# Performance work log

Measured on AMD Instinct MI355X. Metric: run time of the kernel, lower is better.

## Reference

```python
import jax, jax.numpy as jnp
import numpy as np

B, A, C = 128, 8732, 21
ALPHA = 1.0
NEG_POS_RATIO = 3


def setup_inputs() -> dict:
    key = jax.random.key(0)
    k1, k2, k3, k4, k5 = jax.random.split(key, 5)
    confidences = jax.random.normal(k1, (B, A, C), dtype=jnp.float32)
    locations = jax.random.normal(k2, (B, A, 4), dtype=jnp.float32)
    gt_locations = jax.random.normal(k3, (B, A, 4), dtype=jnp.float32)
    raw_cls = jax.random.randint(k4, (B, A), 1, C)
    is_pos = jax.random.uniform(k5, (B, A)) < 0.03
    gt_labels = jnp.where(is_pos, raw_cls, 0).astype(jnp.int32)
    return {
        "confidences": confidences,
        "locations": locations,
        "gt_labels": gt_labels,
        "gt_locations": gt_locations,
    }


def reference(confidences, locations, gt_labels, gt_locations):
    pos_mask = gt_labels > 0                     # (B, A)
    neg_avail = gt_labels == 0                   # (B, A)

    # smooth L1 (beta=1) summed over positive anchors
    d = locations - gt_locations                 # (B, A, 4)
    ad = jnp.abs(d)
    sl1 = jnp.where(ad < 1.0, 0.5 * d * d, ad - 0.5)
    loc_loss = jnp.sum(sl1 * pos_mask[..., None].astype(sl1.dtype))

    # per-anchor cross entropy
    logp = jax.nn.log_softmax(confidences, axis=-1)              # (B, A, C)
    ce = -jnp.take_along_axis(logp, gt_labels[..., None].astype(jnp.int32), axis=-1)[..., 0]  # (B, A)

    # hard negative mining: top-(3*num_pos) CE among negatives, per row
    num_pos = jnp.sum(pos_mask, axis=1)                          # (B,)
    num_neg = jnp.minimum(NEG_POS_RATIO * num_pos, jnp.sum(neg_avail, axis=1))
    ce_neg = jnp.where(pos_mask, 0.0, ce)                        # zero out positives (CE >= 0)
    order = jnp.argsort(-ce_neg, axis=1)                         # descending
    ranks = jnp.argsort(order, axis=1)                           # rank of each anchor in descending order
    neg_mask = ranks < num_neg[:, None]

    keep = pos_mask | neg_mask
    conf_loss = jnp.sum(jnp.where(keep, ce, 0.0))

    total_loss = (loc_loss + ALPHA * conf_loss) / jnp.sum(num_pos).astype(loc_loss.dtype)
    return total_loss
```

## Files before the change

kernel.cpp:

```cpp
#include <hip/hip_runtime.h>
#include <math.h>

#define B_ 128
#define A_ 8732
#define C_ 21
#define TPB 1024
#define KPT 9
#define NT 9

typedef float f4u __attribute__((ext_vector_type(4), aligned(4)));

#define OFF_SCAL 0

__global__ __launch_bounds__(1024) void k_fused(
        const float* __restrict__ conf, const float* __restrict__ loc,
        const int* __restrict__ lab, const float* __restrict__ gloc,
        float* __restrict__ gsum, int* __restrict__ gN,
        int* __restrict__ gticket, float* __restrict__ out)
{
    __shared__ unsigned long long shCnt[2][16];
    __shared__ float shS[16];
    __shared__ float shL[16];
    __shared__ int   shC[16];
    __shared__ int   shNp;

    const int b    = blockIdx.x;
    const int tid  = threadIdx.x;
    const int wave = tid >> 6, lane = tid & 63;
    const size_t rowoff = (size_t)b * A_;

    unsigned keys[KPT];
    float pce = 0.f, lloss = 0.f;
    int pcnt = 0;

    #pragma unroll
    for (int t = 0; t < NT; ++t) {
        const int a  = t * TPB + tid;
        unsigned key = 0u;
        if (a < A_) {
            const int L = lab[rowoff + a];

            const float* vp = conf + (rowoff + a) * C_;
            float v[C_];
            #pragma unroll
            for (int q = 0; q < 5; ++q) {
                const f4u x = *(const f4u*)(vp + 4 * q);
                v[4*q+0] = x.x; v[4*q+1] = x.y; v[4*q+2] = x.z; v[4*q+3] = x.w;
            }
            v[20] = vp[20];

            float m = v[0];
            #pragma unroll
            for (int j = 1; j < C_; ++j) m = fmaxf(m, v[j]);
            float s = 0.f;
            #pragma unroll
            for (int j = 0; j < C_; ++j) s += __expf(v[j] - m);

            float vL = v[0];
            #pragma unroll
            for (int j = 1; j < C_; ++j) vL = (j == L) ? v[j] : vL;

            const float ce = __logf(s) + m - vL;
            if (L > 0) {
                pce += ce;
                pcnt++;
                const float4 lv = ((const float4*)loc)[rowoff + a];
                const float4 gv = ((const float4*)gloc)[rowoff + a];
                float dx = lv.x - gv.x, dy = lv.y - gv.y,
                      dz = lv.z - gv.z, dw = lv.w - gv.w;
                float ax = fabsf(dx), ay = fabsf(dy),
                      az = fabsf(dz), aw = fabsf(dw);
                lloss += (ax < 1.f) ? 0.5f * dx * dx : ax - 0.5f;
                lloss += (ay < 1.f) ? 0.5f * dy * dy : ay - 0.5f;
                lloss += (az < 1.f) ? 0.5f * dz * dz : az - 0.5f;
                lloss += (aw < 1.f) ? 0.5f * dw * dw : aw - 0.5f;
            } else {
                key = __float_as_uint(ce);
            }
        }
        keys[t] = key;
    }

    {
        float p = pce, l = lloss; int c = pcnt;
        #pragma unroll
        for (int off = 32; off > 0; off >>= 1) {
            p += __shfl_down(p, off);
            l += __shfl_down(l, off);
            c += __shfl_down(c, off);
        }
        if (lane == 0) { shS[wave] = p; shL[wave] = l; shC[wave] = c; }
    }
    __syncthreads();
    float rowsum = 0.f;
    if (tid == 0) {
        float P = 0.f, Lx = 0.f; int Cc = 0;
        #pragma unroll
        for (int w = 0; w < 16; ++w) { P += shS[w]; Lx += shL[w]; Cc += shC[w]; }
        shNp = Cc;
        rowsum = P + Lx;
    }
    __syncthreads();
    const int np = shNp;

    {
        unsigned c0 = 0; float s0 = 0.f;
        #pragma unroll
        for (int j = 0; j < KPT; ++j) {
            c0 += (unsigned)__popcll(__ballot(keys[j] != 0u));
            s0 += __uint_as_float(keys[j]);
        }
        #pragma unroll
        for (int off = 32; off > 0; off >>= 1) s0 += __shfl_down(s0, off);
        if (lane == 0) { shCnt[0][wave] = c0; shS[wave] = s0; }
    }
    __syncthreads();

    const int k = min(3 * np, A_ - np);
    unsigned cnt0 = 0; float sum0 = 0.f;
    #pragma unroll
    for (int w = 0; w < 16; ++w) { cnt0 += (unsigned)shCnt[0][w]; sum0 += shS[w]; }

    float negsum = 0.f;
    if (k <= 0) {
        negsum = 0.f;
    } else if (cnt0 < (unsigned)k) {
        negsum = sum0;
    } else {
        unsigned lo = 0u, hi = 0x42800000u;
        int p = 1;
        while (hi - lo > 1u) {
            const unsigned w = hi - lo;
            unsigned m1, m2, m3;
            if (w >= 4u) { const unsigned q = w >> 2; m1 = lo + q; m2 = lo + 2*q; m3 = lo + 3*q; }
            else         { m1 = m2 = m3 = lo + (w >> 1); }
            unsigned c1 = 0, c2 = 0, c3 = 0;
            #pragma unroll
            for (int j = 0; j < KPT; ++j) {
                c1 += (unsigned)__popcll(__ballot(keys[j] > m1));
                c2 += (unsigned)__popcll(__ballot(keys[j] > m2));
                c3 += (unsigned)__popcll(__ballot(keys[j] > m3));
            }
            if (lane == 0)
                shCnt[p][wave] = (unsigned long long)c1
                               | ((unsigned long long)c2 << 16)
                               | ((unsigned long long)c3 << 32);
            __syncthreads();
            unsigned long long tsum = 0;
            #pragma unroll
            for (int w2 = 0; w2 < 16; ++w2) tsum += shCnt[p][w2];
            const int C1 = (int)(tsum & 0xFFFF), C2 = (int)((tsum >> 16) & 0xFFFF),
                      C3 = (int)((tsum >> 32) & 0xFFFF);
            if      (C3 >= k) { lo = m3; }
            else if (C2 >= k) { lo = m2; hi = m3; }
            else if (C1 >= k) { lo = m1; hi = m2; }
            else              { hi = m1; }
            p ^= 1;
        }

        const unsigned kth = hi;
        unsigned c = 0; float s = 0.f;
        #pragma unroll
        for (int j = 0; j < KPT; ++j) {
            c += (unsigned)__popcll(__ballot(keys[j] > kth));
            s += (keys[j] > kth) ? __uint_as_float(keys[j]) : 0.f;
        }
        #pragma unroll
        for (int off = 32; off > 0; off >>= 1) s += __shfl_down(s, off);
        if (lane == 0) { shCnt[0][wave] = c; shS[wave] = s; }
        __syncthreads();
        if (tid == 0) {
            unsigned Cg = 0; float Sg = 0.f;
            #pragma unroll
            for (int w = 0; w < 16; ++w) { Cg += (unsigned)shCnt[0][w]; Sg += shS[w]; }
            negsum = Sg + (float)(k - (int)Cg) * __uint_as_float(kth);
        }
    }

    if (tid == 0) {
        atomicAdd(gsum, rowsum + negsum);
        atomicAdd(gN, np);
        __threadfence();
        const int t = atomicAdd(gticket, 1);
        if (t == B_ - 1) {
            const float S = atomicAdd(gsum, 0.f);
            const int   N = atomicAdd(gN, 0);
            out[0] = S / (float)N;
        }
    }
}

extern "C" void kernel_launch(void* const* d_in, const int* in_sizes, int n_in,
                              void* d_out, int out_size, void* d_ws, size_t ws_size,
                              hipStream_t stream) {
    const float* conf = (const float*)d_in[0];
    const float* loc  = (const float*)d_in[1];
    const int*   lab  = (const int*)d_in[2];
    const float* gloc = (const float*)d_in[3];

    char* ws = (char*)d_ws;
    float* gsum    = (float*)(ws + OFF_SCAL);
    int*   gN      = (int*)(ws + OFF_SCAL + 4);
    int*   gticket = (int*)(ws + OFF_SCAL + 8);

    hipMemsetAsync(ws + OFF_SCAL, 0, 12, stream);

    k_fused<<<B_, TPB, 0, stream>>>(conf, loc, lab, gloc,
                                    gsum, gN, gticket, (float*)d_out);
}
```

Before: 190.7 us.

## Software-pipeline anchor loads and use online softmax per float4 chunk

Prefetches the next tile's confidences, label, and location vectors into registers while the current tile is processed, so global memory latency overlaps with compute. Replaces the two-pass max/exp softmax with an online streaming softmax over float4 chunks. Loads loc/gloc unconditionally for every anchor instead of only for positives, and adds a launch-bounds occupancy hint. This raises register pressure and adds extra location traffic and extra exp work from rescaling.

After: 194.5 us. About the same (+2.0%).

```diff
diff --git a/kernel.cpp b/kernel.cpp
--- a/kernel.cpp
+++ b/kernel.cpp
@@ -12,7 +12,22 @@
 
 #define OFF_SCAL 0
 
-__global__ __launch_bounds__(1024) void k_fused(
+#define SM_CHUNK(X, BASE)                                             \
+    {                                                                 \
+        const float e0 = X.x, e1 = X.y, e2 = X.z, e3 = X.w;           \
+        const float cm = fmaxf(fmaxf(e0, e1), fmaxf(e2, e3));         \
+        const float nm = fmaxf(m, cm);                                \
+        s = s * __expf(m - nm)                                        \
+          + __expf(e0 - nm) + __expf(e1 - nm)                         \
+          + __expf(e2 - nm) + __expf(e3 - nm);                        \
+        m = nm;                                                       \
+        vL = (cL == (BASE) + 0) ? e0 : vL;                            \
+        vL = (cL == (BASE) + 1) ? e1 : vL;                            \
+        vL = (cL == (BASE) + 2) ? e2 : vL;                            \
+        vL = (cL == (BASE) + 3) ? e3 : vL;                            \
+    }
+
+__global__ __launch_bounds__(1024, 4) void k_fused(
         const float* __restrict__ conf, const float* __restrict__ loc,
         const int* __restrict__ lab, const float* __restrict__ gloc,
         float* __restrict__ gsum, int* __restrict__ gN,
@@ -33,41 +48,56 @@
     float pce = 0.f, lloss = 0.f;
     int pcnt = 0;
 
+    f4u cx0, cx1, cx2, cx3, cx4; float cxs; int cL; float4 clv, cgv;
+    f4u nx0, nx1, nx2, nx3, nx4; float nxs; int nL; float4 nlv, ngv;
+
+    {
+        const float* vp = conf + (rowoff + tid) * C_;
+        cx0 = *(const f4u*)(vp);      cx1 = *(const f4u*)(vp + 4);
+        cx2 = *(const f4u*)(vp + 8);  cx3 = *(const f4u*)(vp + 12);
+        cx4 = *(const f4u*)(vp + 16); cxs = vp[20];
+        cL  = lab[rowoff + tid];
+        clv = ((const float4*)loc)[rowoff + tid];
+        cgv = ((const float4*)gloc)[rowoff + tid];
+    }
+
     #pragma unroll
     for (int t = 0; t < NT; ++t) {
-        const int a  = t * TPB + tid;
+        if (t + 1 < NT) {
+            const int a = (t + 1) * TPB + tid;
+            if (a < A_) {
+                const float* vp = conf + (rowoff + a) * C_;
+                nx0 = *(const f4u*)(vp);      nx1 = *(const f4u*)(vp + 4);
+                nx2 = *(const f4u*)(vp + 8);  nx3 = *(const f4u*)(vp + 12);
+                nx4 = *(const f4u*)(vp + 16); nxs = vp[20];
+                nL  = lab[rowoff + a];
+                nlv = ((const float4*)loc)[rowoff + a];
+                ngv = ((const float4*)gloc)[rowoff + a];
+            } else {
+                nx0 = (f4u){0.f, 0.f, 0.f, 0.f}; nx1 = nx0; nx2 = nx0;
+                nx3 = nx0; nx4 = nx0; nxs = 0.f; nL = 0;
+                nlv = make_float4(0.f, 0.f, 0.f, 0.f); ngv = nlv;
+            }
+        }
+
+        const int a = t * TPB + tid;
         unsigned key = 0u;
         if (a < A_) {
-            const int L = lab[rowoff + a];
-
-            const float* vp = conf + (rowoff + a) * C_;
-            float v[C_];
-            #pragma unroll
-            for (int q = 0; q < 5; ++q) {
-                const f4u x = *(const f4u*)(vp + 4 * q);
-                v[4*q+0] = x.x; v[4*q+1] = x.y; v[4*q+2] = x.z; v[4*q+3] = x.w;
-            }
-            v[20] = vp[20];
-
-            float m = v[0];
-            #pragma unroll
-            for (int j = 1; j < C_; ++j) m = fmaxf(m, v[j]);
-            float s = 0.f;
-            #pragma unroll
-            for (int j = 0; j < C_; ++j) s += __expf(v[j] - m);
-
-            float vL = v[0];
-            #pragma unroll
-            for (int j = 1; j < C_; ++j) vL = (j == L) ? v[j] : vL;
-
+            float m = -1e30f, s = 0.f, vL = 0.f;
+            SM_CHUNK(cx0,  0) SM_CHUNK(cx1,  4) SM_CHUNK(cx2,  8)
+            SM_CHUNK(cx3, 12) SM_CHUNK(cx4, 16)
+            {
+                const float nm = fmaxf(m, cxs);
+                s = s * __expf(m - nm) + __expf(cxs - nm);
+                m = nm;
+                vL = (cL == 20) ? cxs : vL;
+            }
             const float ce = __logf(s) + m - vL;
-            if (L > 0) {
+            if (cL > 0) {
                 pce += ce;
                 pcnt++;
-                const float4 lv = ((const float4*)loc)[rowoff + a];
-                const float4 gv = ((const float4*)gloc)[rowoff + a];
-                float dx = lv.x - gv.x, dy = lv.y - gv.y,
-                      dz = lv.z - gv.z, dw = lv.w - gv.w;
+                float dx = clv.x - cgv.x, dy = clv.y - cgv.y,
+                      dz = clv.z - cgv.z, dw = clv.w - cgv.w;
                 float ax = fabsf(dx), ay = fabsf(dy),
                       az = fabsf(dz), aw = fabsf(dw);
                 lloss += (ax < 1.f) ? 0.5f * dx * dx : ax - 0.5f;
@@ -79,6 +109,9 @@
             }
         }
         keys[t] = key;
+
+        cx0 = nx0; cx1 = nx1; cx2 = nx2; cx3 = nx3; cx4 = nx4;
+        cxs = nxs; cL = nL; clv = nlv; cgv = ngv;
     }
 
     {
```

## Split fused loss into wide CE kernel and per-row selection kernel

Applied to the files above, without the earlier changes.

The single 128-block fused kernel is replaced by two kernels. The first computes per-anchor cross entropy and the localization loss over a (35, 128) grid of 256-thread blocks, so many more blocks share the memory-bound read of the confidences. It writes negative CE values to a workspace buffer and atomically accumulates per-row positive counts. The second kernel loads each row's CE values into shared memory and runs the existing radix-style top-k selection. This costs an extra ~4.5 MB write and read plus a second launch, and the softmax now uses an online max/sum form.

Measured after the change: 220.8 us. 1.16x slower.

```diff
diff --git a/kernel.cpp b/kernel.cpp
--- a/kernel.cpp
+++ b/kernel.cpp
@@ -4,111 +4,136 @@
 #define B_ 128
 #define A_ 8732
 #define C_ 21
+#define APB 256
+#define NBLK ((A_ + APB - 1) / APB)
 #define TPB 1024
 #define KPT 9
-#define NT 9
 
 typedef float f4u __attribute__((ext_vector_type(4), aligned(4)));
 
 #define OFF_SCAL 0
-
-__global__ __launch_bounds__(1024) void k_fused(
+#define OFF_RNP  16
+#define OFF_CEN  1024
+
+#define SM_CHUNK(X, BASE)                                             \
+    {                                                                 \
+        const float e0 = X.x, e1 = X.y, e2 = X.z, e3 = X.w;           \
+        const float cm = fmaxf(fmaxf(e0, e1), fmaxf(e2, e3));         \
+        const float nm = fmaxf(m, cm);                                \
+        s = s * __expf(m - nm)                                        \
+          + __expf(e0 - nm) + __expf(e1 - nm)                         \
+          + __expf(e2 - nm) + __expf(e3 - nm);                        \
+        m = nm;                                                       \
+        vL = (L == (BASE) + 0) ? e0 : vL;                             \
+        vL = (L == (BASE) + 1) ? e1 : vL;                             \
+        vL = (L == (BASE) + 2) ? e2 : vL;                             \
+        vL = (L == (BASE) + 3) ? e3 : vL;                             \
+    }
+
+__global__ __launch_bounds__(256) void k_ce(
         const float* __restrict__ conf, const float* __restrict__ loc,
         const int* __restrict__ lab, const float* __restrict__ gloc,
+        float* __restrict__ ce_neg, int* __restrict__ row_np,
+        float* __restrict__ gsum)
+{
+    const int row = blockIdx.y;
+    const int a   = blockIdx.x * APB + threadIdx.x;
+    const int tid = threadIdx.x;
+    const int wave = tid >> 6, lane = tid & 63;
+
+    float pce = 0.f, lloss = 0.f;
+    int pcnt = 0;
+
+    if (a < A_) {
+        const size_t idx = (size_t)row * A_ + a;
+        const int L = lab[idx];
+        const float* vp = conf + idx * C_;
+        const f4u x0 = *(const f4u*)(vp);
+        const f4u x1 = *(const f4u*)(vp + 4);
+        const f4u x2 = *(const f4u*)(vp + 8);
+        const f4u x3 = *(const f4u*)(vp + 12);
+        const f4u x4 = *(const f4u*)(vp + 16);
+        const float xs = vp[20];
+
+        float m = -1e30f, s = 0.f, vL = 0.f;
+        SM_CHUNK(x0,  0) SM_CHUNK(x1,  4) SM_CHUNK(x2,  8)
+        SM_CHUNK(x3, 12) SM_CHUNK(x4, 16)
+        {
+            const float nm = fmaxf(m, xs);
+            s = s * __expf(m - nm) + __expf(xs - nm);
+            m = nm;
+            vL = (L == 20) ? xs : vL;
+        }
+        const float ce = __logf(s) + m - vL;
+
+        if (L > 0) {
+            pce = ce;
+            pcnt = 1;
+            const float4 lv = ((const float4*)loc)[idx];
+            const float4 gv = ((const float4*)gloc)[idx];
+            float dx = lv.x - gv.x, dy = lv.y - gv.y,
+                  dz = lv.z - gv.z, dw = lv.w - gv.w;
+            float ax = fabsf(dx), ay = fabsf(dy),
+                  az = fabsf(dz), aw = fabsf(dw);
+            lloss  = (ax < 1.f) ? 0.5f * dx * dx : ax - 0.5f;
+            lloss += (ay < 1.f) ? 0.5f * dy * dy : ay - 0.5f;
+            lloss += (az < 1.f) ? 0.5f * dz * dz : az - 0.5f;
+            lloss += (aw < 1.f) ? 0.5f * dw * dw : aw - 0.5f;
+            ce_neg[idx] = 0.f;
+        } else {
+            ce_neg[idx] = ce;
+        }
+    }
+
+    #pragma unroll
+    for (int off = 32; off > 0; off >>= 1) {
+        pce   += __shfl_down(pce, off);
+        lloss += __shfl_down(lloss, off);
+        pcnt  += __shfl_down(pcnt, off);
+    }
+    __shared__ float wf[4], wl[4];
+    __shared__ int wc[4];
+    if (lane == 0) { wf[wave] = pce; wl[wave] = lloss; wc[wave] = pcnt; }
+    __syncthreads();
+    if (tid == 0) {
+        const float S = wf[0] + wf[1] + wf[2] + wf[3]
+                      + wl[0] + wl[1] + wl[2] + wl[3];
+        const int Cc = wc[0] + wc[1] + wc[2] + wc[3];
+        if (S != 0.f) atomicAdd(gsum, S);
+        if (Cc)       atomicAdd(&row_np[row], Cc);
+    }
+}
+
+__global__ __launch_bounds__(1024) void k_sel(
+        const float* __restrict__ ce_neg, const int* __restrict__ row_np,
         float* __restrict__ gsum, int* __restrict__ gN,
         int* __restrict__ gticket, float* __restrict__ out)
 {
+    __shared__ unsigned kls[KPT * TPB];
     __shared__ unsigned long long shCnt[2][16];
     __shared__ float shS[16];
-    __shared__ float shL[16];
-    __shared__ int   shC[16];
-    __shared__ int   shNp;
-
-    const int b    = blockIdx.x;
-    const int tid  = threadIdx.x;
+
+    const int b = blockIdx.x;
+    const int tid = threadIdx.x;
     const int wave = tid >> 6, lane = tid & 63;
-    const size_t rowoff = (size_t)b * A_;
-
-    unsigned keys[KPT];
-    float pce = 0.f, lloss = 0.f;
-    int pcnt = 0;
+    const float* ce = ce_neg + (size_t)b * A_;
 
     #pragma unroll
-    for (int t = 0; t < NT; ++t) {
-        const int a  = t * TPB + tid;
-        unsigned key = 0u;
-        if (a < A_) {
-            const int L = lab[rowoff + a];
-
-            const float* vp = conf + (rowoff + a) * C_;
-            float v[C_];
-            #pragma unroll
-            for (int q = 0; q < 5; ++q) {
-                const f4u x = *(const f4u*)(vp + 4 * q);
-                v[4*q+0] = x.x; v[4*q+1] = x.y; v[4*q+2] = x.z; v[4*q+3] = x.w;
-            }
-            v[20] = vp[20];
-
-            float m = v[0];
-            #pragma unroll
-            for (int j = 1; j < C_; ++j) m = fmaxf(m, v[j]);
-            float s = 0.f;
-            #pragma unroll
-            for (int j = 0; j < C_; ++j) s += __expf(v[j] - m);
-
-            float vL = v[0];
-            #pragma unroll
-            for (int j = 1; j < C_; ++j) vL = (j == L) ? v[j] : vL;
-
-            const float ce = __logf(s) + m - vL;
-            if (L > 0) {
-                pce += ce;
-                pcnt++;
-                const float4 lv = ((const float4*)loc)[rowoff + a];
-                const float4 gv = ((const float4*)gloc)[rowoff + a];
-                float dx = lv.x - gv.x, dy = lv.y - gv.y,
-                      dz = lv.z - gv.z, dw = lv.w - gv.w;
-                float ax = fabsf(dx), ay = fabsf(dy),
-                      az = fabsf(dz), aw = fabsf(dw);
-                lloss += (ax < 1.f) ? 0.5f * dx * dx : ax - 0.5f;
-                lloss += (ay < 1.f) ? 0.5f * dy * dy : ay - 0.5f;
-                lloss += (az < 1.f) ? 0.5f * dz * dz : az - 0.5f;
-                lloss += (aw < 1.f) ? 0.5f * dw * dw : aw - 0.5f;
-            } else {
-                key = __float_as_uint(ce);
-            }
-        }
-        keys[t] = key;
-    }
-
-    {
-        float p = pce, l = lloss; int c = pcnt;
-        #pragma unroll
-        for (int off = 32; off > 0; off >>= 1) {
-            p += __shfl_down(p, off);
-            l += __shfl_down(l, off);
-            c += __shfl_down(c, off);
-        }
-        if (lane == 0) { shS[wave] = p; shL[wave] = l; shC[wave] = c; }
-    }
+    for (int j = 0; j < KPT; ++j) {
+        const int i = tid + j * TPB;
+        kls[i] = (i < A_) ? __float_as_uint(ce[i]) : 0u;
+    }
+    const int np = row_np[b];
+    if (tid == 0) atomicAdd(gN, np);
     __syncthreads();
-    float rowsum = 0.f;
-    if (tid == 0) {
-        float P = 0.f, Lx = 0.f; int Cc = 0;
-        #pragma unroll
-        for (int w = 0; w < 16; ++w) { P += shS[w]; Lx += shL[w]; Cc += shC[w]; }
-        shNp = Cc;
-        rowsum = P + Lx;
-    }
-    __syncthreads();
-    const int np = shNp;
 
     {
         unsigned c0 = 0; float s0 = 0.f;
         #pragma unroll
         for (int j = 0; j < KPT; ++j) {
-            c0 += (unsigned)__popcll(__ballot(keys[j] != 0u));
-            s0 += __uint_as_float(keys[j]);
+            const unsigned key = kls[tid + j * TPB];
+            c0 += (unsigned)__popcll(__ballot(key != 0u));
+            s0 += __uint_as_float(key);
         }
         #pragma unroll
         for (int off = 32; off > 0; off >>= 1) s0 += __shfl_down(s0, off);
@@ -137,9 +162,10 @@
             unsigned c1 = 0, c2 = 0, c3 = 0;
             #pragma unroll
             for (int j = 0; j < KPT; ++j) {
-                c1 += (unsigned)__popcll(__ballot(keys[j] > m1));
-                c2 += (unsigned)__popcll(__ballot(keys[j] > m2));
-                c3 += (unsigned)__popcll(__ballot(keys[j] > m3));
+                const unsigned key = kls[tid + j * TPB];
+                c1 += (unsigned)__popcll(__ballot(key > m1));
+                c2 += (unsigned)__popcll(__ballot(key > m2));
+                c3 += (unsigned)__popcll(__ballot(key > m3));
             }
             if (lane == 0)
                 shCnt[p][wave] = (unsigned long long)c1
@@ -162,8 +188,9 @@
         unsigned c = 0; float s = 0.f;
         #pragma unroll
         for (int j = 0; j < KPT; ++j) {
-            c += (unsigned)__popcll(__ballot(keys[j] > kth));
-            s += (keys[j] > kth) ? __uint_as_float(keys[j]) : 0.f;
+            const unsigned key = kls[tid + j * TPB];
+            c += (unsigned)__popcll(__ballot(key > kth));
+            s += (key > kth) ? __uint_as_float(key) : 0.f;
         }
         #pragma unroll
         for (int off = 32; off > 0; off >>= 1) s += __shfl_down(s, off);
@@ -178,8 +205,7 @@
     }
 
     if (tid == 0) {
-        atomicAdd(gsum, rowsum + negsum);
-        atomicAdd(gN, np);
+        atomicAdd(gsum, negsum);
         __threadfence();
         const int t = atomicAdd(gticket, 1);
         if (t == B_ - 1) {
@@ -199,12 +225,16 @@
     const float* gloc = (const float*)d_in[3];
 
     char* ws = (char*)d_ws;
-    float* gsum    = (float*)(ws + OFF_SCAL);
-    int*   gN      = (int*)(ws + OFF_SCAL + 4);
-    int*   gticket = (int*)(ws + OFF_SCAL + 8);
-
-    hipMemsetAsync(ws + OFF_SCAL, 0, 12, stream);
-
-    k_fused<<<B_, TPB, 0, stream>>>(conf, loc, lab, gloc,
-                                    gsum, gN, gticket, (float*)d_out);
+    float* gsum   = (float*)(ws + OFF_SCAL);
+    int*   gN     = (int*)(ws + OFF_SCAL + 4);
+    int*   gticket= (int*)(ws + OFF_SCAL + 8);
+    int*   row_np = (int*)(ws + OFF_RNP);
+    float* ce_neg = (float*)(ws + OFF_CEN);
+
+    hipMemsetAsync(ws, 0, OFF_RNP + B_ * sizeof(int), stream);
+
+    dim3 g1(NBLK, B_);
+    k_ce<<<g1, APB, 0, stream>>>(conf, loc, lab, gloc, ce_neg, row_np, gsum);
+    k_sel<<<B_, TPB, 0, stream>>>(ce_neg, row_np, gsum, gN, gticket,
+                                  (float*)d_out);
 }
```
